# Kernel tuning notes

Hardware: AMD Instinct MI355X
Metric: run time of the kernel (lower is better)

The kernel has to match this reference:

```python
import jax, jax.numpy as jnp
import numpy as np

B, NA, F, K, L = 96, 48, 128, 64, 6
CUT = 5.0


def _forward(pos, f_in, emb, msg_w1, msg_b1, msg_w2, msg_b2, rbf_w, rbf_b,
             upd_U, upd_V, upd_w1, upd_b1, upd_w2, upd_b2,
             out_w1, out_b1, out_w2, out_b2, node_atom):
    p = pos.reshape(B, NA, 3)
    rij = p[:, :, None, :] - p[:, None, :, :]          # [B,n,n,3], pos_i - pos_j
    d2 = jnp.sum(rij * rij, -1)
    eye = jnp.eye(NA, dtype=bool)
    d = jnp.sqrt(jnp.where(eye, 1.0, d2))              # safe sqrt on diagonal
    mask = (~eye) & (d < CUT)                          # radius_graph, loop=False
    centers = jnp.linspace(0.0, CUT, K)
    gamma = 1.0 / ((CUT / K) ** 2 + 1e-9)
    rbf = jnp.exp(-gamma * (d[..., None] - centers) ** 2)   # [B,n,n,K]
    cutf = 0.5 * (jnp.cos(jnp.pi * d / CUT) + 1.0)          # cosine cutoff
    w_env = jnp.where(mask, cutf, 0.0)[..., None]
    dirv = rij / d[..., None]                               # unit directions
    s = emb[node_atom].reshape(B, NA, F)
    v = jnp.zeros((B, NA, 3, F), s.dtype)
    for l in range(L):
        # message block
        phi = jax.nn.silu(s @ msg_w1[l] + msg_b1[l]) @ msg_w2[l] + msg_b2[l]  # [B,n,3F]
        Wf = (rbf @ rbf_w[l] + rbf_b[l]) * w_env                              # [B,n,n,3F]
        x = phi[:, None, :, :] * Wf                                           # phi of sender j
        ds, dvv, dvs = jnp.split(x, 3, axis=-1)
        s = s + ds.sum(2)
        v = v + jnp.einsum('bijf,bjcf->bicf', dvv, v) \
              + jnp.einsum('bijf,bijc->bicf', dvs, dirv)
        # update block
        Uv = jnp.einsum('bncf,fg->bncg', v, upd_U[l])
        Vv = jnp.einsum('bncf,fg->bncg', v, upd_V[l])
        Vn = jnp.sqrt(jnp.sum(Vv * Vv, 2) + 1e-8)                             # [B,n,F]
        a = jax.nn.silu(jnp.concatenate([s, Vn], -1) @ upd_w1[l] + upd_b1[l]) @ upd_w2[l] + upd_b2[l]
        avv, asv, ass = jnp.split(a, 3, -1)
        v = v + avv[:, :, None, :] * Uv
        s = s + asv * jnp.sum(Uv * Vv, 2) + ass
    out = jax.nn.silu(s @ out_w1 + out_b1) @ out_w2 + out_b2                  # [B,n,1]
    return out.sum(1)                                                         # per-graph sum


def setup_inputs() -> dict:
    key = jax.random.key(0)
    ks = jax.random.split(key, 16)
    N = B * NA
    pos = jax.random.normal(ks[0], (N, 3), jnp.float32) * 2.0
    f_in = jnp.zeros((N, 1), jnp.float32)
    node_atom = jax.random.randint(ks[1], (N,), 1, 84)
    batch = jnp.arange(N) // NA
    g = lambda k, shp, fan: jax.random.normal(k, shp, jnp.float32) / np.sqrt(fan)
    return dict(
        f_in=f_in, pos=pos, batch=batch, node_atom=node_atom,
        emb=g(ks[2], (100, F), 1.0),
        msg_w1=g(ks[3], (L, F, F), F), msg_b1=jnp.zeros((L, F), jnp.float32),
        msg_w2=g(ks[4], (L, F, 3 * F), F), msg_b2=jnp.zeros((L, 3 * F), jnp.float32),
        rbf_w=g(ks[5], (L, K, 3 * F), K), rbf_b=jnp.zeros((L, 3 * F), jnp.float32),
        upd_U=g(ks[6], (L, F, F), F), upd_V=g(ks[7], (L, F, F), F),
        upd_w1=g(ks[8], (L, 2 * F, F), 2 * F), upd_b1=jnp.zeros((L, F), jnp.float32),
        upd_w2=g(ks[9], (L, F, 3 * F), F), upd_b2=jnp.zeros((L, 3 * F), jnp.float32),
        out_w1=g(ks[10], (F, F), F), out_b1=jnp.zeros((F,), jnp.float32),
        out_w2=g(ks[11], (F, 1), F), out_b2=jnp.zeros((1,), jnp.float32),
    )


def reference(f_in, pos, batch, node_atom, emb, msg_w1, msg_b1, msg_w2, msg_b2,
              rbf_w, rbf_b, upd_U, upd_V, upd_w1, upd_b1, upd_w2, upd_b2,
              out_w1, out_b1, out_w2, out_b2):
    return _forward(pos, f_in, emb, msg_w1, msg_b1, msg_w2, msg_b2, rbf_w, rbf_b,
                    upd_U, upd_V, upd_w1, upd_b1, upd_w2, upd_b2,
                    out_w1, out_b1, out_w2, out_b2, node_atom)
```

## Files before the change

### kernel.cpp

```cpp
#include <hip/hip_runtime.h>
#include <math.h>

#define NB 96
#define NA 48
#define NF 128
#define NK 64
#define NL 6
#define NN (NB*NA)
#define F3 (3*NF)
#define CUTF 5.0f
#define GAMMA_F ((float)(1.0 / (0.006103515625 + 1e-9)))
#define PI_F 3.14159265358979323846f

typedef __attribute__((ext_vector_type(8))) short short8;
typedef __attribute__((ext_vector_type(4))) float floatx4;
typedef __attribute__((ext_vector_type(2))) float floatx2;

#define LO2(v) __builtin_shufflevector(v, v, 0, 1)
#define HI2(v) __builtin_shufflevector(v, v, 2, 3)

#define PHX(g, mt, ff, jl) (((((size_t)(g))*3 + (mt))*384 + (ff))*16 + (jl))

__device__ __forceinline__ float silu_f(float x) { return x / (1.0f + expf(-x)); }

__device__ __forceinline__ short f2bf(float x) {
    unsigned u = __builtin_bit_cast(unsigned, x);
    unsigned r = (u + 0x7fffu + ((u >> 16) & 1u)) >> 16;
    return (short)r;
}
__device__ __forceinline__ float bf2f(short h) {
    unsigned u = ((unsigned)(unsigned short)h) << 16;
    return __builtin_bit_cast(float, u);
}
__device__ __forceinline__ floatx4 mfma1(short8 a, short8 b, floatx4 c) {
    return __builtin_amdgcn_mfma_f32_16x16x32_bf16(a, b, c, 0, 0, 0);
}
__device__ __forceinline__ floatx4 mfma3(short8 ah, short8 al, short8 bh, short8 bl, floatx4 c) {
    c = __builtin_amdgcn_mfma_f32_16x16x32_bf16(ah, bh, c, 0, 0, 0);
    c = __builtin_amdgcn_mfma_f32_16x16x32_bf16(al, bh, c, 0, 0, 0);
    c = __builtin_amdgcn_mfma_f32_16x16x32_bf16(ah, bl, c, 0, 0, 0);
    return c;
}

__global__ void prep_kernel(const float* __restrict__ msg_w1, const float* __restrict__ msg_w2,
                            const float* __restrict__ rbf_w, const float* __restrict__ upd_U,
                            const float* __restrict__ upd_V, const float* __restrict__ upd_w1,
                            const float* __restrict__ upd_w2,
                            short* w1T_h, short* w1T_l, short* w2T_h, short* w2T_l,
                            short* rbfT_h, short* rbfT_l, short* UT_h, short* UT_l,
                            short* VT_h, short* VT_l, short* u1T_h, short* u1T_l,
                            short* u2T_h, short* u2T_l) {
    int m = blockIdx.y;
    int l = blockIdx.x / 384;
    int n = blockIdx.x % 384;
    const float* src; short* dh; short* dl; int K, N;
    switch (m) {
      case 0: src = msg_w1; dh = w1T_h; dl = w1T_l; K = NF;   N = NF; break;
      case 1: src = msg_w2; dh = w2T_h; dl = w2T_l; K = NF;   N = F3; break;
      case 2: src = rbf_w;  dh = rbfT_h;dl = rbfT_l;K = NK;   N = F3; break;
      case 3: src = upd_U;  dh = UT_h;  dl = UT_l;  K = NF;   N = NF; break;
      case 4: src = upd_V;  dh = VT_h;  dl = VT_l;  K = NF;   N = NF; break;
      case 5: src = upd_w1; dh = u1T_h; dl = u1T_l; K = 2*NF; N = NF; break;
      default:src = upd_w2; dh = u2T_h; dl = u2T_l; K = NF;   N = F3; break;
    }
    if (n >= N) return;
    for (int k = threadIdx.x; k < K; k += 64) {
        float x = src[((size_t)l*K + k)*N + n];
        short h = f2bf(x);
        size_t off = (size_t)l*N*K
                   + (size_t)((((n>>4)*(K>>5) + (k>>5))*4 + ((k>>3)&3))*128 + (n&15)*8 + (k&7));
        dh[off] = h;
        dl[off] = f2bf(x - bf2f(h));
    }
}

__global__ void __launch_bounds__(256) geom_kernel(const float* __restrict__ pos,
                                                   float* __restrict__ weG,
                                                   float* __restrict__ dirG,
                                                   short* __restrict__ rbfP) {
    int e = blockIdx.x*256 + threadIdx.x;
    int i = e / NA, j = e % NA;
    int b = i / NA, il = i % NA;
    int jg = b*NA + j;
    float dx = pos[i*3+0] - pos[jg*3+0];
    float dy = pos[i*3+1] - pos[jg*3+1];
    float dz = pos[i*3+2] - pos[jg*3+2];
    float d2 = dx*dx + dy*dy + dz*dz;
    float dd = sqrtf((j == il) ? 1.0f : d2);
    bool valid = (j != il) && (dd < CUTF);
    float we = valid ? 0.5f*(cosf(PI_F * dd / CUTF) + 1.0f) : 0.0f;
    weG[e] = we;
    float inv = 1.0f / dd;
    dirG[0*(size_t)NN*NA + e] = dx*inv;
    dirG[1*(size_t)NN*NA + e] = dy*inv;
    dirG[2*(size_t)NN*NA + e] = dz*inv;
    int mt = j >> 4, colj = j & 15;
    size_t rb = (size_t)i*3072 + (size_t)(mt*2)*512 + (size_t)colj*8;
    #pragma unroll
    for (int half = 0; half < 2; ++half) {
        #pragma unroll
        for (int c = 0; c < 4; ++c) {
            short8 h8;
            #pragma unroll
            for (int kk = 0; kk < 8; ++kk) {
                int k = half*32 + c*8 + kk;
                float cen = CUTF * (float)k / 63.0f;
                float df = dd - cen;
                h8[kk] = f2bf(__expf(-GAMMA_F * df * df) * we);
            }
            *(short8*)&rbfP[rb + half*512 + c*128] = h8;
        }
    }
}

__global__ void zero_kernel(float* __restrict__ p) {
    p[(size_t)blockIdx.x * blockDim.x + threadIdx.x] = 0.f;
}

__global__ void __launch_bounds__(128) init_phi_kernel(
        const float* __restrict__ emb, const int* __restrict__ node_atom,
        const short* __restrict__ w1T_h, const short* __restrict__ w1T_l,
        const float* __restrict__ b1,
        const short* __restrict__ w2T_h, const short* __restrict__ w2T_l,
        const float* __restrict__ b2,
        float* __restrict__ s, float* __restrict__ v, float* __restrict__ phiX) {
    __shared__ short sH[16*NF], sL[16*NF];
    __shared__ short hH[16*NF], hL[16*NF];
    int t = threadIdx.x;
    int w = t >> 6, lane = t & 63, quad = lane >> 4, col = lane & 15;
    int n0 = blockIdx.x * 16;
    int g = n0 / NA, mt0 = (n0 % NA) >> 4;
    for (int e = t; e < 16*NF; e += 128) {
        int n = e >> 7, f = e & 127;
        int a = node_atom[n0+n];
        float x = emb[(size_t)a*NF + f];
        s[(size_t)(n0+n)*NF + f] = x;
        short h = f2bf(x);
        int ad = n*NF + (((f >> 3) ^ (n & 7)) << 3) + (f & 7);
        sH[ad] = h; sL[ad] = f2bf(x - bf2f(h));
    }
    for (int e = t; e < 16*F3; e += 128) v[(size_t)n0*F3 + e] = 0.f;
    __syncthreads();
    #pragma unroll
    for (int nt = 0; nt < 4; ++nt) {
        int fh = w*64 + nt*16 + col;
        floatx4 acc = (floatx4){0.f,0.f,0.f,0.f};
        #pragma unroll
        for (int ks = 0; ks < 4; ++ks) {
            int ad = col*NF + (((ks*4 + quad) ^ (col & 7)) << 3);
            size_t off = (size_t)((((w*4 + nt)*4 + ks)*4 + quad)*128) + col*8;
            acc = mfma3(*(short8*)&sH[ad], *(short8*)&sL[ad],
                        *(const short8*)(w1T_h + off), *(const short8*)(w1T_l + off), acc);
        }
        float bias = b1[fh];
        #pragma unroll
        for (int r = 0; r < 4; ++r) {
            int n = quad*4 + r;
            float hv = silu_f(acc[r] + bias);
            short h = f2bf(hv);
            int ad = n*NF + (((fh >> 3) ^ (n & 7)) << 3) + (fh & 7);
            hH[ad] = h; hL[ad] = f2bf(hv - bf2f(h));
        }
    }
    __syncthreads();
    #pragma unroll
    for (int nt = 0; nt < 12; ++nt) {
        int tt = w*192 + nt*16 + col;
        floatx4 acc = (floatx4){0.f,0.f,0.f,0.f};
        #pragma unroll
        for (int ks = 0; ks < 4; ++ks) {
            int ad = col*NF + (((ks*4 + quad) ^ (col & 7)) << 3);
            size_t off = (size_t)((((w*12 + nt)*4 + ks)*4 + quad)*128) + col*8;
            acc = mfma3(*(short8*)&hH[ad], *(short8*)&hL[ad],
                        *(const short8*)(w2T_h + off), *(const short8*)(w2T_l + off), acc);
        }
        float bias = b2[tt];
        floatx4 o;
        #pragma unroll
        for (int r = 0; r < 4; ++r) o[r] = acc[r] + bias;
        *(floatx4*)(phiX + PHX(g, mt0, tt, quad*4)) = o;
    }
}

__global__ void __launch_bounds__(512, 2) message_kernel(
        const float* __restrict__ sIn, const float* __restrict__ vIn,
        const float* __restrict__ phiX, const float* __restrict__ vX,
        const float* __restrict__ weG, const float* __restrict__ dirG,
        const short* __restrict__ rbfP,
        const short* __restrict__ rbfT_h,
        const float* __restrict__ rbf_b_l,
        float* __restrict__ sOut, float* __restrict__ vOut) {
    __shared__ short tkL[36*512];
    __shared__ float weL[6][NA];
    __shared__ float dirL[3][6][NA];
    int raw = blockIdx.x;
    int xcd = raw & 7, idx = raw >> 3;
    int graph = xcd + 8*(idx % 12);
    int itile = idx / 12;
    int i0l = itile*6, jbase = graph*NA;
    int n0 = jbase + i0l;
    int t = threadIdx.x;
    int w = t >> 6, lane = t & 63, quad = lane >> 4, col = lane & 15;
    int f = w*16 + col;
    float rb0 = rbf_b_l[f], rb1 = rbf_b_l[NF+f], rb2 = rbf_b_l[2*NF+f];
    floatx2 rb0v = {rb0, rb0}, rb1v = {rb1, rb1}, rb2v = {rb2, rb2};
    short8 B[3][2];
    #pragma unroll
    for (int g = 0; g < 3; ++g)
        #pragma unroll
        for (int ks = 0; ks < 2; ++ks)
            B[g][ks] = *(const short8*)(rbfT_h + (size_t)((((g*8 + w)*2 + ks)*4 + quad)*128) + col*8);
    {
        const short8* rs = (const short8*)(rbfP + (size_t)n0*3072);
        short8* rd = (short8*)tkL;
        for (int u = t; u < 2304; u += 512) rd[u] = rs[u];
        if (t < 288) {
            int ii = t / NA, j = t % NA;
            size_t e = (size_t)(n0 + ii)*NA + j;
            weL[ii][j] = weG[e];
            dirL[0][ii][j] = dirG[0*(size_t)NN*NA + e];
            dirL[1][ii][j] = dirG[1*(size_t)NN*NA + e];
            dirL[2][ii][j] = dirG[2*(size_t)NN*NA + e];
        }
    }
    __syncthreads();
    float accS[6], av0[6], av1[6], av2[6];
    #pragma unroll
    for (int ia = 0; ia < 6; ++ia) { accS[ia]=0.f; av0[ia]=0.f; av1[ia]=0.f; av2[ia]=0.f; }
    #pragma unroll 1
    for (int mt = 0; mt < 3; ++mt) {
        int jq = quad*4;
        floatx4 p0 = *(const floatx4*)(phiX + PHX(graph, mt, f, jq));
        floatx4 p1 = *(const floatx4*)(phiX + PHX(graph, mt, NF+f, jq));
        floatx4 p2 = *(const floatx4*)(phiX + PHX(graph, mt, 2*NF+f, jq));
        floatx4 u0 = *(const floatx4*)(vX + PHX(graph, mt, 0*NF+f, jq));
        floatx4 u1 = *(const floatx4*)(vX + PHX(graph, mt, 1*NF+f, jq));
        floatx4 u2 = *(const floatx4*)(vX + PHX(graph, mt, 2*NF+f, jq));
        int jl = mt*16 + quad*4;
        #pragma unroll
        for (int ia = 0; ia < 6; ++ia) {
            floatx4 C0 = (floatx4){0.f,0.f,0.f,0.f};
            floatx4 C1 = (floatx4){0.f,0.f,0.f,0.f};
            floatx4 C2 = (floatx4){0.f,0.f,0.f,0.f};
            #pragma unroll
            for (int ks = 0; ks < 2; ++ks) {
                short8 a = *(short8*)&tkL[(((ia*3 + mt)*2 + ks) << 9) + lane*8];
                C0 = mfma1(a, B[0][ks], C0);
                C1 = mfma1(a, B[1][ks], C1);
                C2 = mfma1(a, B[2][ks], C2);
            }
            floatx4 we4 = *(const floatx4*)&weL[ia][jl];
            floatx4 d0 = *(const floatx4*)&dirL[0][ia][jl];
            floatx4 d1 = *(const floatx4*)&dirL[1][ia][jl];
            floatx4 d2 = *(const floatx4*)&dirL[2][ia][jl];
            floatx2 aS = {0.f,0.f}, a0 = {0.f,0.f}, a1 = {0.f,0.f}, a2 = {0.f,0.f};
            {
                floatx2 we2 = LO2(we4);
                floatx2 Wf0 = rb0v*we2 + LO2(C0);
                aS += LO2(p0) * Wf0;
                floatx2 Wf1 = rb1v*we2 + LO2(C1);
                floatx2 x1 = LO2(p1) * Wf1;
                a0 += x1 * LO2(u0);
                a1 += x1 * LO2(u1);
                a2 += x1 * LO2(u2);
                floatx2 Wf2 = rb2v*we2 + LO2(C2);
                floatx2 x2 = LO2(p2) * Wf2;
                a0 += x2 * LO2(d0);
                a1 += x2 * LO2(d1);
                a2 += x2 * LO2(d2);
            }
            {
                floatx2 we2 = HI2(we4);
                floatx2 Wf0 = rb0v*we2 + HI2(C0);
                aS += HI2(p0) * Wf0;
                floatx2 Wf1 = rb1v*we2 + HI2(C1);
                floatx2 x1 = HI2(p1) * Wf1;
                a0 += x1 * HI2(u0);
                a1 += x1 * HI2(u1);
                a2 += x1 * HI2(u2);
                floatx2 Wf2 = rb2v*we2 + HI2(C2);
                floatx2 x2 = HI2(p2) * Wf2;
                a0 += x2 * HI2(d0);
                a1 += x2 * HI2(d1);
                a2 += x2 * HI2(d2);
            }
            accS[ia] += aS.x + aS.y;
            av0[ia]  += a0.x + a0.y;
            av1[ia]  += a1.x + a1.y;
            av2[ia]  += a2.x + a2.y;
        }
    }
    #pragma unroll
    for (int ia = 0; ia < 6; ++ia) {
        int i = n0 + ia;
        float aS = accS[ia], A0 = av0[ia], A1 = av1[ia], A2 = av2[ia];
        aS += __shfl_xor(aS, 16, 64); aS += __shfl_xor(aS, 32, 64);
        A0 += __shfl_xor(A0, 16, 64); A0 += __shfl_xor(A0, 32, 64);
        A1 += __shfl_xor(A1, 16, 64); A1 += __shfl_xor(A1, 32, 64);
        A2 += __shfl_xor(A2, 16, 64); A2 += __shfl_xor(A2, 32, 64);
        if (quad == 0) {
            sOut[(size_t)i*NF + f]        = sIn[(size_t)i*NF + f]        + aS;
            vOut[(size_t)i*F3 + f]        = vIn[(size_t)i*F3 + f]        + A0;
            vOut[(size_t)i*F3 + NF + f]   = vIn[(size_t)i*F3 + NF + f]   + A1;
            vOut[(size_t)i*F3 + 2*NF + f] = vIn[(size_t)i*F3 + 2*NF + f] + A2;
        }
    }
}

__global__ void __launch_bounds__(512) update_phi_kernel(
        const short* __restrict__ UT_h, const short* __restrict__ VT_h,
        const short* __restrict__ u1T_h, const float* __restrict__ b1,
        const short* __restrict__ u2T_h, const float* __restrict__ b2,
        float* __restrict__ s, float* __restrict__ v, float* __restrict__ vX,
        int doPhi,
        const short* __restrict__ pw1_h, const float* __restrict__ pb1,
        const short* __restrict__ pw2_h, const float* __restrict__ pb2,
        float* __restrict__ phiX) {
    __shared__ short A1h[48*NF], A1l[48*NF];
    __shared__ short A2h[16*256];
    __shared__ short hH[16*NF];
    __shared__ float sF[6*132];
    int t = threadIdx.x;
    int w = t >> 6, lane = t & 63, quad = lane >> 4, col = lane & 15;
    int raw = blockIdx.x;
    int xcd = raw & 7, idx = raw >> 3;
    int graph = xcd + 8*(idx % 12);
    int jb0 = (idx / 12)*6;
    int n0 = graph*NA + jb0;
    int f = w*16 + col;
    for (int e = t; e < 6*F3; e += 512) {
        int n = e / F3, cf = e % F3;
        int c = cf >> 7, ff = cf & 127;
        float x = v[(size_t)(n0+n)*F3 + cf];
        int row = c*16 + n;
        short h = f2bf(x);
        int ad = row*NF + (((ff >> 3) ^ (row & 7)) << 3) + (ff & 7);
        A1h[ad] = h; A1l[ad] = f2bf(x - bf2f(h));
    }
    for (int e = t; e < 6*NF; e += 512) {
        int n = e >> 7, ff = e & 127;
        float x = s[(size_t)(n0+n)*NF + ff];
        sF[n*132 + ff] = x;
        int ad = n*256 + (((ff >> 3) ^ (n & 7)) << 3) + (ff & 7);
        A2h[ad] = f2bf(x);
    }
    __syncthreads();
    floatx4 Uacc[3], Vacc[3];
    #pragma unroll
    for (int mt = 0; mt < 3; ++mt) { Uacc[mt] = (floatx4){0.f,0.f,0.f,0.f}; Vacc[mt] = (floatx4){0.f,0.f,0.f,0.f}; }
    #pragma unroll
    for (int ks = 0; ks < 4; ++ks) {
        size_t off = (size_t)(((w*4 + ks)*4 + quad)*128) + col*8;
        short8 BU = *(const short8*)(UT_h + off);
        short8 BV = *(const short8*)(VT_h + off);
        #pragma unroll
        for (int mt = 0; mt < 3; ++mt) {
            int row = mt*16 + col;
            int ad = row*NF + (((ks*4 + quad) ^ (row & 7)) << 3);
            short8 ah = *(short8*)&A1h[ad];
            Uacc[mt] = mfma1(ah, BU, Uacc[mt]);
            Vacc[mt] = mfma1(ah, BV, Vacc[mt]);
        }
    }
    if (quad < 2) {
        #pragma unroll
        for (int r = 0; r < 4; ++r) {
            int n = quad*4 + r;
            if (n < 6) {
                float v0 = Vacc[0][r], v1 = Vacc[1][r], v2 = Vacc[2][r];
                float vn = sqrtf(v0*v0 + v1*v1 + v2*v2 + 1e-8f);
                int ad = n*256 + ((((128 + f) >> 3) ^ (n & 7)) << 3) + (f & 7);
                A2h[ad] = f2bf(vn);
            }
        }
    }
    __syncthreads();
    {
        floatx4 H = (floatx4){0.f,0.f,0.f,0.f};
        #pragma unroll
        for (int ks = 0; ks < 8; ++ks) {
            int ad = col*256 + (((ks*4 + quad) ^ (col & 7)) << 3);
            short8 ah = *(short8*)&A2h[ad];
            size_t off = (size_t)(((w*8 + ks)*4 + quad)*128) + col*8;
            H = mfma1(ah, *(const short8*)(u1T_h + off), H);
        }
        float bias = b1[f];
        if (quad < 2) {
            #pragma unroll
            for (int r = 0; r < 4; ++r) {
                int n = quad*4 + r;
                if (n < 6) {
                    float hv = silu_f(H[r] + bias);
                    int ad = n*NF + (((f >> 3) ^ (n & 7)) << 3) + (f & 7);
                    hH[ad] = f2bf(hv);
                }
            }
        }
    }
    __syncthreads();
    floatx4 O[3];
    #pragma unroll
    for (int gg = 0; gg < 3; ++gg) O[gg] = (floatx4){0.f,0.f,0.f,0.f};
    #pragma unroll
    for (int ks = 0; ks < 4; ++ks) {
        int ad = col*NF + (((ks*4 + quad) ^ (col & 7)) << 3);
        short8 ah = *(short8*)&hH[ad];
        #pragma unroll
        for (int gg = 0; gg < 3; ++gg) {
            size_t off = (size_t)((((gg*8 + w)*4 + ks)*4 + quad)*128) + col*8;
            O[gg] = mfma1(ah, *(const short8*)(u2T_h + off), O[gg]);
        }
    }
    __syncthreads();
    short* pH = A2h;
    if (quad < 2) {
        float bavv = b2[f], basv = b2[NF + f], bass = b2[2*NF + f];
        #pragma unroll
        for (int r = 0; r < 4; ++r) {
            int n = quad*4 + r;
            if (n < 6) {
                float avv = O[0][r] + bavv;
                float asv = O[1][r] + basv;
                float ass = O[2][r] + bass;
                float dot = Uacc[0][r]*Vacc[0][r] + Uacc[1][r]*Vacc[1][r] + Uacc[2][r]*Vacc[2][r];
                float snew = sF[n*132 + f] + asv*dot + ass;
                s[(size_t)(n0+n)*NF + f] = snew;
                int adS = n*NF + (((f >> 3) ^ (n & 7)) << 3) + (f & 7);
                pH[adS] = f2bf(snew);
                int jl = jb0 + n;
                int mtt = jl >> 4, jl16 = jl & 15;
                #pragma unroll
                for (int c = 0; c < 3; ++c) {
                    int row = c*16 + n;
                    int ad = row*NF + (((f >> 3) ^ (row & 7)) << 3) + (f & 7);
                    float vold = bf2f(A1h[ad]) + bf2f(A1l[ad]);
                    float vnew = vold + avv*Uacc[c][r];
                    v[(size_t)(n0+n)*F3 + c*NF + f] = vnew;
                    vX[PHX(graph, mtt, c*NF + f, jl16)] = vnew;
                }
            }
        }
    }
    if (!doPhi) return;
    __syncthreads();
    {
        floatx4 acc = (floatx4){0.f,0.f,0.f,0.f};
        #pragma unroll
        for (int ks = 0; ks < 4; ++ks) {
            int ad = col*NF + (((ks*4 + quad) ^ (col & 7)) << 3);
            size_t off = (size_t)(((w*4 + ks)*4 + quad)*128) + col*8;
            acc = mfma1(*(short8*)&pH[ad], *(const short8*)(pw1_h + off), acc);
        }
        float bias = pb1[f];
        if (quad < 2) {
            #pragma unroll
            for (int r = 0; r < 4; ++r) {
                int n = quad*4 + r;
                if (n < 6) {
                    float hv = silu_f(acc[r] + bias);
                    int ad = n*NF + (((f >> 3) ^ (n & 7)) << 3) + (f & 7);
                    hH[ad] = f2bf(hv);
                }
            }
        }
    }
    __syncthreads();
    #pragma unroll
    for (int nt = 0; nt < 3; ++nt) {
        int tt = (w*3 + nt)*16 + col;
        floatx4 acc = (floatx4){0.f,0.f,0.f,0.f};
        #pragma unroll
        for (int ks = 0; ks < 4; ++ks) {
            int ad = col*NF + (((ks*4 + quad) ^ (col & 7)) << 3);
            size_t off = (size_t)((((w*3 + nt)*4 + ks)*4 + quad)*128) + col*8;
            acc = mfma1(*(short8*)&hH[ad], *(const short8*)(pw2_h + off), acc);
        }
        float bias = pb2[tt];
        if (quad < 2) {
            #pragma unroll
            for (int r = 0; r < 4; ++r) {
                int no = quad*4 + r;
                if (no < 6) {
                    int jl = jb0 + no;
                    int mtt = jl >> 4, jl16 = jl & 15;
                    phiX[PHX(graph, mtt, tt, jl16)] = acc[r] + bias;
                }
            }
        }
    }
}

__global__ void zero_out_kernel(float* __restrict__ out) {
    out[threadIdx.x] = 0.f;
}

__global__ void out_kernel(const float* __restrict__ s,
                           const float* __restrict__ w1, const float* __restrict__ b1,
                           const float* __restrict__ w2, const float* __restrict__ b2,
                           float* __restrict__ out) {
    int n = blockIdx.x;
    int f = threadIdx.x;
    __shared__ float sh[NF];
    __shared__ float r2[2];
    sh[f] = s[n*NF + f];
    __syncthreads();
    float acc = b1[f];
    for (int g = 0; g < NF; ++g) acc = fmaf(sh[g], w1[g*NF + f], acc);
    float p = silu_f(acc) * w2[f];
    #pragma unroll
    for (int off = 32; off > 0; off >>= 1) p += __shfl_down(p, off, 64);
    if ((f & 63) == 0) r2[f >> 6] = p;
    __syncthreads();
    if (f == 0) atomicAdd(&out[n / NA], r2[0] + r2[1] + b2[0]);
}

extern "C" void kernel_launch(void* const* d_in, const int* in_sizes, int n_in,
                              void* d_out, int out_size, void* d_ws, size_t ws_size,
                              hipStream_t stream) {
    (void)in_sizes; (void)n_in; (void)out_size; (void)ws_size;
    const float* pos      = (const float*)d_in[1];
    const int*   node_atom= (const int*)  d_in[3];
    const float* emb      = (const float*)d_in[4];
    const float* msg_w1   = (const float*)d_in[5];
    const float* msg_b1   = (const float*)d_in[6];
    const float* msg_w2   = (const float*)d_in[7];
    const float* msg_b2   = (const float*)d_in[8];
    const float* rbf_w    = (const float*)d_in[9];
    const float* rbf_b    = (const float*)d_in[10];
    const float* upd_U    = (const float*)d_in[11];
    const float* upd_V    = (const float*)d_in[12];
    const float* upd_w1   = (const float*)d_in[13];
    const float* upd_b1   = (const float*)d_in[14];
    const float* upd_w2   = (const float*)d_in[15];
    const float* upd_b2   = (const float*)d_in[16];
    const float* out_w1   = (const float*)d_in[17];
    const float* out_b1   = (const float*)d_in[18];
    const float* out_w2   = (const float*)d_in[19];
    const float* out_b2   = (const float*)d_in[20];
    float* out = (float*)d_out;

    float* ws   = (float*)d_ws;
    float* sA   = ws; ws += (size_t)NN*NF;
    float* sB   = ws; ws += (size_t)NN*NF;
    float* vA   = ws; ws += (size_t)NN*F3;
    float* vB   = ws; ws += (size_t)NN*F3;
    float* phiX = ws; ws += (size_t)F3*NN;
    float* vX   = ws; ws += (size_t)F3*NN;
    float* weG  = ws; ws += (size_t)NN*NA;
    float* dirG = ws; ws += (size_t)3*NN*NA;
    short* sp    = (short*)ws;
    short* rbfP  = sp; sp += (size_t)NN*3072;
    short* w1T_h = sp; sp += (size_t)NL*NF*NF;
    short* w1T_l = sp; sp += (size_t)NL*NF*NF;
    short* w2T_h = sp; sp += (size_t)NL*F3*NF;
    short* w2T_l = sp; sp += (size_t)NL*F3*NF;
    short* rbfT_h= sp; sp += (size_t)NL*F3*NK;
    short* rbfT_l= sp; sp += (size_t)NL*F3*NK;
    short* UT_h  = sp; sp += (size_t)NL*NF*NF;
    short* UT_l  = sp; sp += (size_t)NL*NF*NF;
    short* VT_h  = sp; sp += (size_t)NL*NF*NF;
    short* VT_l  = sp; sp += (size_t)NL*NF*NF;
    short* u1T_h = sp; sp += (size_t)NL*NF*2*NF;
    short* u1T_l = sp; sp += (size_t)NL*NF*2*NF;
    short* u2T_h = sp; sp += (size_t)NL*F3*NF;
    short* u2T_l = sp; sp += (size_t)NL*F3*NF;

    prep_kernel<<<dim3(NL*384, 7), 64, 0, stream>>>(msg_w1, msg_w2, rbf_w, upd_U, upd_V, upd_w1, upd_w2,
                                                    w1T_h, w1T_l, w2T_h, w2T_l, rbfT_h, rbfT_l,
                                                    UT_h, UT_l, VT_h, VT_l, u1T_h, u1T_l, u2T_h, u2T_l);
    geom_kernel<<<(NN*NA)/256, 256, 0, stream>>>(pos, weG, dirG, rbfP);
    zero_kernel<<<(F3*NN)/256, 256, 0, stream>>>(vX);
    init_phi_kernel<<<NN/16, 128, 0, stream>>>(emb, node_atom,
                                               w1T_h, w1T_l, msg_b1, w2T_h, w2T_l, msg_b2,
                                               sA, vA, phiX);

    float* sC = sA; float* vC = vA; float* sN = sB; float* vN = vB;
    for (int l = 0; l < NL; ++l) {
        message_kernel<<<NB*8, 512, 0, stream>>>(sC, vC, phiX, vX,
                                                 weG, dirG, rbfP,
                                                 rbfT_h + (size_t)l*F3*NK,
                                                 rbf_b + (size_t)l*F3, sN, vN);
        int lp = (l + 1 < NL) ? (l + 1) : 0;
        update_phi_kernel<<<NN/6, 512, 0, stream>>>(
            UT_h + (size_t)l*NF*NF, VT_h + (size_t)l*NF*NF,
            u1T_h + (size_t)l*NF*2*NF, upd_b1 + (size_t)l*NF,
            u2T_h + (size_t)l*F3*NF, upd_b2 + (size_t)l*F3,
            sN, vN, vX,
            (l + 1 < NL) ? 1 : 0,
            w1T_h + (size_t)lp*NF*NF, msg_b1 + (size_t)lp*NF,
            w2T_h + (size_t)lp*F3*NF, msg_b2 + (size_t)lp*F3,
            phiX);
        float* tp;
        tp = sC; sC = sN; sN = tp;
        tp = vC; vC = vN; vN = tp;
    }
    zero_out_kernel<<<1, NB, 0, stream>>>(out);
    out_kernel<<<NN, NF, 0, stream>>>(sC, out_w1, out_b1, out_w2, out_b2, out);
}
```

Measured before the change: 537.3 us.

## Fuse message and update/phi kernels into one per-layer kernel

Merges the message kernel and the update/phi kernel into a single kernel per layer. The message results are handed straight to the update stage through shared memory, so the intermediate s/v no longer round-trip through global memory and one launch per layer goes away. phiX and vX are double-buffered so the next layer's inputs can be written while other blocks still read the current ones, and s/v are updated in place. Shared memory is aliased between the two phases and launch bounds rise to 3 blocks per CU, which may add register pressure.

```diff
diff --git a/kernel.cpp b/kernel.cpp
--- a/kernel.cpp
+++ b/kernel.cpp
@@ -182,26 +182,39 @@
     }
 }
 
-__global__ void __launch_bounds__(512, 2) message_kernel(
-        const float* __restrict__ sIn, const float* __restrict__ vIn,
-        const float* __restrict__ phiX, const float* __restrict__ vX,
+__global__ void __launch_bounds__(512, 3) fused_layer_kernel(
+        float* __restrict__ s, float* __restrict__ v,
+        const float* __restrict__ phiXin, const float* __restrict__ vXin,
         const float* __restrict__ weG, const float* __restrict__ dirG,
         const short* __restrict__ rbfP,
-        const short* __restrict__ rbfT_h,
-        const float* __restrict__ rbf_b_l,
-        float* __restrict__ sOut, float* __restrict__ vOut) {
-    __shared__ short tkL[36*512];
-    __shared__ float weL[6][NA];
-    __shared__ float dirL[3][6][NA];
+        const short* __restrict__ rbfT_h, const float* __restrict__ rbf_b_l,
+        const short* __restrict__ UT_h, const short* __restrict__ VT_h,
+        const short* __restrict__ u1T_h, const float* __restrict__ b1,
+        const short* __restrict__ u2T_h, const float* __restrict__ b2,
+        int doPhi,
+        const short* __restrict__ pw1_h, const float* __restrict__ pb1,
+        const short* __restrict__ pw2_h, const float* __restrict__ pb2,
+        float* __restrict__ phiXout, float* __restrict__ vXout) {
+    __shared__ __align__(16) char SM[41472];
+    short* tkL = (short*)SM;
+    float (*weL)[NA] = (float (*)[NA])(SM + 36864);
+    float (*dirL)[6][NA] = (float (*)[6][NA])(SM + 38016);
+    short* A1h = (short*)SM;
+    short* A1l = (short*)(SM + 12288);
+    short* A2h = (short*)(SM + 24576);
+    short* hH  = (short*)(SM + 32768);
+    float* sF  = (float*)(SM + 36864);
+
     int raw = blockIdx.x;
     int xcd = raw & 7, idx = raw >> 3;
     int graph = xcd + 8*(idx % 12);
     int itile = idx / 12;
-    int i0l = itile*6, jbase = graph*NA;
-    int n0 = jbase + i0l;
+    int i0l = itile*6;
+    int n0 = graph*NA + i0l;
     int t = threadIdx.x;
     int w = t >> 6, lane = t & 63, quad = lane >> 4, col = lane & 15;
     int f = w*16 + col;
+
     float rb0 = rbf_b_l[f], rb1 = rbf_b_l[NF+f], rb2 = rbf_b_l[2*NF+f];
     floatx2 rb0v = {rb0, rb0}, rb1v = {rb1, rb1}, rb2v = {rb2, rb2};
     short8 B[3][2];
@@ -230,12 +243,12 @@
     #pragma unroll 1
     for (int mt = 0; mt < 3; ++mt) {
         int jq = quad*4;
-        floatx4 p0 = *(const floatx4*)(phiX + PHX(graph, mt, f, jq));
-        floatx4 p1 = *(const floatx4*)(phiX + PHX(graph, mt, NF+f, jq));
-        floatx4 p2 = *(const floatx4*)(phiX + PHX(graph, mt, 2*NF+f, jq));
-        floatx4 u0 = *(const floatx4*)(vX + PHX(graph, mt, 0*NF+f, jq));
-        floatx4 u1 = *(const floatx4*)(vX + PHX(graph, mt, 1*NF+f, jq));
-        floatx4 u2 = *(const floatx4*)(vX + PHX(graph, mt, 2*NF+f, jq));
+        floatx4 p0 = *(const floatx4*)(phiXin + PHX(graph, mt, f, jq));
+        floatx4 p1 = *(const floatx4*)(phiXin + PHX(graph, mt, NF+f, jq));
+        floatx4 p2 = *(const floatx4*)(phiXin + PHX(graph, mt, 2*NF+f, jq));
+        floatx4 u0 = *(const floatx4*)(vXin + PHX(graph, mt, 0*NF+f, jq));
+        floatx4 u1 = *(const floatx4*)(vXin + PHX(graph, mt, 1*NF+f, jq));
+        floatx4 u2 = *(const floatx4*)(vXin + PHX(graph, mt, 2*NF+f, jq));
         int jl = mt*16 + quad*4;
         #pragma unroll
         for (int ia = 0; ia < 6; ++ia) {
@@ -292,59 +305,35 @@
     }
     #pragma unroll
     for (int ia = 0; ia < 6; ++ia) {
-        int i = n0 + ia;
-        float aS = accS[ia], A0 = av0[ia], A1 = av1[ia], A2 = av2[ia];
-        aS += __shfl_xor(aS, 16, 64); aS += __shfl_xor(aS, 32, 64);
-        A0 += __shfl_xor(A0, 16, 64); A0 += __shfl_xor(A0, 32, 64);
-        A1 += __shfl_xor(A1, 16, 64); A1 += __shfl_xor(A1, 32, 64);
-        A2 += __shfl_xor(A2, 16, 64); A2 += __shfl_xor(A2, 32, 64);
-        if (quad == 0) {
-            sOut[(size_t)i*NF + f]        = sIn[(size_t)i*NF + f]        + aS;
-            vOut[(size_t)i*F3 + f]        = vIn[(size_t)i*F3 + f]        + A0;
-            vOut[(size_t)i*F3 + NF + f]   = vIn[(size_t)i*F3 + NF + f]   + A1;
-            vOut[(size_t)i*F3 + 2*NF + f] = vIn[(size_t)i*F3 + 2*NF + f] + A2;
-        }
-    }
-}
-
-__global__ void __launch_bounds__(512) update_phi_kernel(
-        const short* __restrict__ UT_h, const short* __restrict__ VT_h,
-        const short* __restrict__ u1T_h, const float* __restrict__ b1,
-        const short* __restrict__ u2T_h, const float* __restrict__ b2,
-        float* __restrict__ s, float* __restrict__ v, float* __restrict__ vX,
-        int doPhi,
-        const short* __restrict__ pw1_h, const float* __restrict__ pb1,
-        const short* __restrict__ pw2_h, const float* __restrict__ pb2,
-        float* __restrict__ phiX) {
-    __shared__ short A1h[48*NF], A1l[48*NF];
-    __shared__ short A2h[16*256];
-    __shared__ short hH[16*NF];
-    __shared__ float sF[6*132];
-    int t = threadIdx.x;
-    int w = t >> 6, lane = t & 63, quad = lane >> 4, col = lane & 15;
-    int raw = blockIdx.x;
-    int xcd = raw & 7, idx = raw >> 3;
-    int graph = xcd + 8*(idx % 12);
-    int jb0 = (idx / 12)*6;
-    int n0 = graph*NA + jb0;
-    int f = w*16 + col;
-    for (int e = t; e < 6*F3; e += 512) {
-        int n = e / F3, cf = e % F3;
-        int c = cf >> 7, ff = cf & 127;
-        float x = v[(size_t)(n0+n)*F3 + cf];
-        int row = c*16 + n;
-        short h = f2bf(x);
-        int ad = row*NF + (((ff >> 3) ^ (row & 7)) << 3) + (ff & 7);
-        A1h[ad] = h; A1l[ad] = f2bf(x - bf2f(h));
-    }
-    for (int e = t; e < 6*NF; e += 512) {
-        int n = e >> 7, ff = e & 127;
-        float x = s[(size_t)(n0+n)*NF + ff];
-        sF[n*132 + ff] = x;
-        int ad = n*256 + (((ff >> 3) ^ (n & 7)) << 3) + (ff & 7);
-        A2h[ad] = f2bf(x);
-    }
-    __syncthreads();
+        accS[ia] += __shfl_xor(accS[ia], 16, 64); accS[ia] += __shfl_xor(accS[ia], 32, 64);
+        av0[ia]  += __shfl_xor(av0[ia], 16, 64);  av0[ia]  += __shfl_xor(av0[ia], 32, 64);
+        av1[ia]  += __shfl_xor(av1[ia], 16, 64);  av1[ia]  += __shfl_xor(av1[ia], 32, 64);
+        av2[ia]  += __shfl_xor(av2[ia], 16, 64);  av2[ia]  += __shfl_xor(av2[ia], 32, 64);
+    }
+    __syncthreads();
+
+#define BRIDGE(IA) do { \
+    int i_ = n0 + (IA); \
+    float snew_ = s[(size_t)i_*NF + f] + accS[(IA)]; \
+    sF[(IA)*132 + f] = snew_; \
+    A2h[(IA)*256 + (((f >> 3) ^ ((IA) & 7)) << 3) + (f & 7)] = f2bf(snew_); \
+    { float vn_ = v[(size_t)i_*F3 + 0*NF + f] + av0[(IA)]; int row_ = 0*16 + (IA); \
+      int ad_ = row_*NF + (((f >> 3) ^ (row_ & 7)) << 3) + (f & 7); \
+      short hh_ = f2bf(vn_); A1h[ad_] = hh_; A1l[ad_] = f2bf(vn_ - bf2f(hh_)); } \
+    { float vn_ = v[(size_t)i_*F3 + 1*NF + f] + av1[(IA)]; int row_ = 1*16 + (IA); \
+      int ad_ = row_*NF + (((f >> 3) ^ (row_ & 7)) << 3) + (f & 7); \
+      short hh_ = f2bf(vn_); A1h[ad_] = hh_; A1l[ad_] = f2bf(vn_ - bf2f(hh_)); } \
+    { float vn_ = v[(size_t)i_*F3 + 2*NF + f] + av2[(IA)]; int row_ = 2*16 + (IA); \
+      int ad_ = row_*NF + (((f >> 3) ^ (row_ & 7)) << 3) + (f & 7); \
+      short hh_ = f2bf(vn_); A1h[ad_] = hh_; A1l[ad_] = f2bf(vn_ - bf2f(hh_)); } \
+} while (0)
+    if (quad == 0)      { BRIDGE(0); BRIDGE(4); }
+    else if (quad == 1) { BRIDGE(1); BRIDGE(5); }
+    else if (quad == 2) { BRIDGE(2); }
+    else                { BRIDGE(3); }
+#undef BRIDGE
+    __syncthreads();
+
     floatx4 Uacc[3], Vacc[3];
     #pragma unroll
     for (int mt = 0; mt < 3; ++mt) { Uacc[mt] = (floatx4){0.f,0.f,0.f,0.f}; Vacc[mt] = (floatx4){0.f,0.f,0.f,0.f}; }
@@ -427,7 +416,7 @@
                 s[(size_t)(n0+n)*NF + f] = snew;
                 int adS = n*NF + (((f >> 3) ^ (n & 7)) << 3) + (f & 7);
                 pH[adS] = f2bf(snew);
-                int jl = jb0 + n;
+                int jl = i0l + n;
                 int mtt = jl >> 4, jl16 = jl & 15;
                 #pragma unroll
                 for (int c = 0; c < 3; ++c) {
@@ -436,7 +425,7 @@
                     float vold = bf2f(A1h[ad]) + bf2f(A1l[ad]);
                     float vnew = vold + avv*Uacc[c][r];
                     v[(size_t)(n0+n)*F3 + c*NF + f] = vnew;
-                    vX[PHX(graph, mtt, c*NF + f, jl16)] = vnew;
+                    vXout[PHX(graph, mtt, c*NF + f, jl16)] = vnew;
                 }
             }
         }
@@ -481,9 +470,9 @@
             for (int r = 0; r < 4; ++r) {
                 int no = quad*4 + r;
                 if (no < 6) {
-                    int jl = jb0 + no;
+                    int jl = i0l + no;
                     int mtt = jl >> 4, jl16 = jl & 15;
-                    phiX[PHX(graph, mtt, tt, jl16)] = acc[r] + bias;
+                    phiXout[PHX(graph, mtt, tt, jl16)] = acc[r] + bias;
                 }
             }
         }
@@ -541,11 +530,11 @@
 
     float* ws   = (float*)d_ws;
     float* sA   = ws; ws += (size_t)NN*NF;
-    float* sB   = ws; ws += (size_t)NN*NF;
     float* vA   = ws; ws += (size_t)NN*F3;
-    float* vB   = ws; ws += (size_t)NN*F3;
-    float* phiX = ws; ws += (size_t)F3*NN;
-    float* vX   = ws; ws += (size_t)F3*NN;
+    float* phiXa= ws; ws += (size_t)F3*NN;
+    float* phiXb= ws; ws += (size_t)F3*NN;
+    float* vXa  = ws; ws += (size_t)F3*NN;
+    float* vXb  = ws; ws += (size_t)F3*NN;
     float* weG  = ws; ws += (size_t)NN*NA;
     float* dirG = ws; ws += (size_t)3*NN*NA;
     short* sp    = (short*)ws;
@@ -569,31 +558,29 @@
                                                     w1T_h, w1T_l, w2T_h, w2T_l, rbfT_h, rbfT_l,
                                                     UT_h, UT_l, VT_h, VT_l, u1T_h, u1T_l, u2T_h, u2T_l);
     geom_kernel<<<(NN*NA)/256, 256, 0, stream>>>(pos, weG, dirG, rbfP);
-    zero_kernel<<<(F3*NN)/256, 256, 0, stream>>>(vX);
+    zero_kernel<<<(F3*NN)/256, 256, 0, stream>>>(vXa);
     init_phi_kernel<<<NN/16, 128, 0, stream>>>(emb, node_atom,
                                                w1T_h, w1T_l, msg_b1, w2T_h, w2T_l, msg_b2,
-                                               sA, vA, phiX);
-
-    float* sC = sA; float* vC = vA; float* sN = sB; float* vN = vB;
+                                               sA, vA, phiXa);
+
+    float* phin = phiXa; float* phout = phiXb;
+    float* vxin = vXa;   float* vxout = vXb;
     for (int l = 0; l < NL; ++l) {
-        message_kernel<<<NB*8, 512, 0, stream>>>(sC, vC, phiX, vX,
-                                                 weG, dirG, rbfP,
-                                                 rbfT_h + (size_t)l*F3*NK,
-                                                 rbf_b + (size_t)l*F3, sN, vN);
         int lp = (l + 1 < NL) ? (l + 1) : 0;
-        update_phi_kernel<<<NN/6, 512, 0, stream>>>(
+        fused_layer_kernel<<<NB*8, 512, 0, stream>>>(
+            sA, vA, phin, vxin, weG, dirG, rbfP,
+            rbfT_h + (size_t)l*F3*NK, rbf_b + (size_t)l*F3,
             UT_h + (size_t)l*NF*NF, VT_h + (size_t)l*NF*NF,
             u1T_h + (size_t)l*NF*2*NF, upd_b1 + (size_t)l*NF,
             u2T_h + (size_t)l*F3*NF, upd_b2 + (size_t)l*F3,
-            sN, vN, vX,
             (l + 1 < NL) ? 1 : 0,
             w1T_h + (size_t)lp*NF*NF, msg_b1 + (size_t)lp*NF,
             w2T_h + (size_t)lp*F3*NF, msg_b2 + (size_t)lp*F3,
-            phiX);
+            phout, vxout);
         float* tp;
-        tp = sC; sC = sN; sN = tp;
-        tp = vC; vC = vN; vN = tp;
+        tp = phin; phin = phout; phout = tp;
+        tp = vxin; vxin = vxout; vxout = tp;
     }
     zero_out_kernel<<<1, NB, 0, stream>>>(out);
-    out_kernel<<<NN, NF, 0, stream>>>(sC, out_w1, out_b1, out_w2, out_b2, out);
-}
+    out_kernel<<<NN, NF, 0, stream>>>(sA, out_w1, out_b1, out_w2, out_b2, out);
+}
```

Measured after the change: 571.9 us. 6.4% more time.
